# Performance work log

Hardware: AMD Instinct MI355X
Metric: run time of the kernel (lower is better)

The kernel has to match this reference:

```python
import jax, jax.numpy as jnp
import numpy as np
from jax import lax

N, OC, IC, K = 32, 256, 256, 3
H = W = 56
STRIDE = 1
PADDING = 1
SPARSITY = 0.9  # fraction of zero weights


def setup_inputs() -> dict:
    key = jax.random.key(0)
    k_in, k_w, k_b, k_m = jax.random.split(key, 4)
    input = jax.random.normal(k_in, (N, IC, H, W), dtype=jnp.float32)
    weight = jax.random.normal(k_w, (OC, IC, K, K), dtype=jnp.float32) * 0.05
    bias = jax.random.normal(k_b, (OC,), dtype=jnp.float32) * 0.05
    mask = jax.random.bernoulli(k_m, p=1.0 - SPARSITY, shape=(OC, IC, K, K))
    return {"input": input, "weight": weight, "bias": bias, "mask": mask}


def reference(input, weight, bias, mask):
    # SparseConv2d stores only nonzero weights (W_val at W_idx); mathematically this
    # is a dense conv2d with the masked weight tensor.
    w = jnp.where(mask, weight, jnp.zeros((), dtype=weight.dtype))
    out = lax.conv_general_dilated(
        input, w,
        window_strides=(STRIDE, STRIDE),
        padding=[(PADDING, PADDING), (PADDING, PADDING)],
        dimension_numbers=("NCHW", "OIHW", "NCHW"),
    )
    return out + bias[None, :, None, None]
```

## Files before the change

kernel.cpp:

```cpp
#include <hip/hip_runtime.h>

constexpr int NB=32, ICC=256, OCC=256, HH=56, WW=56;
constexpr int HW=HH*WW, CHW=ICC*HW;
constexpr int YT=14;
constexpr int BUFB = 6*58*64;
constexpr int ROWB = 58*64;
constexpr int LROW=58;
constexpr int PAD=36;
constexpr int LDS_ELEMS=6*LROW*PAD;

using short8  = __attribute__((ext_vector_type(8))) short;
using short4v = __attribute__((ext_vector_type(4))) short;
using f32x4   = __attribute__((ext_vector_type(4))) float;

__device__ inline unsigned bf16rne(float x){
  unsigned u = __float_as_uint(x);
  return (u + 0x7fffu + ((u>>16)&1u)) >> 16;
}

__global__ __launch_bounds__(256) void pack_weights(
    const float* __restrict__ w, const int* __restrict__ mask,
    unsigned short* __restrict__ wb){
  const int oc = blockIdx.x, ic = threadIdx.x;
  const int base = (oc*ICC + ic)*9;
  #pragma unroll
  for (int j=0;j<9;++j){
    float v = (mask[base+j] != 0) ? w[base+j] : 0.f;
    wb[(j*OCC + oc)*ICC + ic] = (unsigned short)bf16rne(v);
  }
}

__global__ __launch_bounds__(256) void pack_input(
    const float* __restrict__ in, unsigned short* __restrict__ inb){
  __shared__ unsigned short t[56*258];
  const int bid = blockIdx.x;
  const int n = bid/56, y = bid - n*56;
  const float* src = in + (size_t)n*CHW + y*WW;
  const int tid = threadIdx.x;
  #pragma unroll
  for (int i=0;i<14;++i){
    int idx = tid + i*256;
    int ic = idx / 14, xg = idx - ic*14;
    float4 v = *(const float4*)(src + ic*HW + xg*4);
    int xb = xg*4;
    t[(xb+0)*258 + ic] = (unsigned short)bf16rne(v.x);
    t[(xb+1)*258 + ic] = (unsigned short)bf16rne(v.y);
    t[(xb+2)*258 + ic] = (unsigned short)bf16rne(v.z);
    t[(xb+3)*258 + ic] = (unsigned short)bf16rne(v.w);
  }
  __syncthreads();
  unsigned* dst = (unsigned*)(inb + (size_t)(n*56+y)*56*256);
  #pragma unroll
  for (int i=0;i<28;++i){
    int idx = tid + i*256;
    int x = idx >> 7, icp = idx & 127;
    dst[idx] = *(const unsigned*)&t[x*258 + icp*2];
  }
}

__global__ __launch_bounds__(256,2) void conv_mfma(
    const unsigned short* __restrict__ inb, const unsigned short* __restrict__ wb,
    const float* __restrict__ bias, float* __restrict__ out){
  __shared__ unsigned short xt[2*6*58*32];

  const int lid  = blockIdx.x;
  const int xcd  = lid & 7, slot = lid >> 3;
  const int ngrp = slot / 28, rem = slot - ngrp*28;
  const int mt   = rem / 14,  yt  = rem - mt*14;
  const int n    = xcd + 8*ngrp;
  const int y0   = yt*4, ocb = mt*128;

  const int tid  = threadIdx.x;
  const int lane = tid & 63, wv = tid >> 6;
  const int q    = lane >> 4, l16 = lane & 15;

  const int ocw = ocb + (wv & 1)*64;
  const int pxw = (wv >> 1)*112;

  int base2[7][3];
  #pragma unroll
  for (int p=0;p<7;++p){
    int px = pxw + p*16 + l16;
    int yl = px / 56, x = px - yl*56;
    #pragma unroll
    for (int kw=0;kw<3;++kw){
      int c = x + kw;
      base2[p][kw] = yl*ROWB + c*64 + ((q ^ ((c>>1)&3))<<4);
    }
  }

  f32x4 acc[4][7];
  #pragma unroll
  for (int s=0;s<4;++s)
    #pragma unroll
    for (int p=0;p<7;++p) acc[s][p] = (f32x4){0.f,0.f,0.f,0.f};

  const int rskipA = (yt==0)      ? 0 : -1;
  const int rskipB = (yt==YT-1)   ? 5 : -1;

  const unsigned short* nb = inb + (size_t)n*(56*56*256);

  auto stage = [&](int buf, int ch){
    const int ic0 = ch*32;
    #pragma unroll
    for (int i=0;i<6;++i){
      int t   = wv*6 + i;
      int row = t >> 2, k = t & 3;
      if (row != rskipA && row != rskipB){
        int ir = k*64 + lane;
        int cc = ir >> 2, sub = ir & 3;
        int icg = sub ^ (((cc+1)>>1)&3);
        int y  = y0 - 1 + row;
        const unsigned short* gp = nb + (y*56 + cc)*256 + ic0 + icg*8;
        char* lp = (char*)xt + buf*BUFB + (row*58 + 1)*64 + k*1024 + lane*16;
        if (ir < 224)
          __builtin_amdgcn_global_load_lds(
              (const __attribute__((address_space(1))) void*)gp,
              (__attribute__((address_space(3))) void*)lp, 16, 0, 0);
      }
    }
  };

  auto compute = [&](int buf, int ch){
    const int ic0 = ch*32;
    const char* xb = (const char*)xt + buf*BUFB;
    const unsigned short* wpb = wb + (ocw + l16)*ICC + ic0 + q*8;
    short8 a0 = *(const short8*)(wpb          );
    short8 a1 = *(const short8*)(wpb + 16*ICC );
    short8 a2 = *(const short8*)(wpb + 32*ICC );
    short8 a3 = *(const short8*)(wpb + 48*ICC );
    __builtin_amdgcn_s_setprio(1);
    #pragma unroll
    for (int j=0;j<9;++j){
      short8 n0, n1, n2, n3;
      if (j < 8){
        const unsigned short* wn = wpb + (j+1)*OCC*ICC;
        n0 = *(const short8*)(wn          );
        n1 = *(const short8*)(wn + 16*ICC );
        n2 = *(const short8*)(wn + 32*ICC );
        n3 = *(const short8*)(wn + 48*ICC );
      }
      const int kh = j/3, kw = j - kh*3;
      const int doff = kh*ROWB;
      #pragma unroll
      for (int p=0;p<7;++p){
        short8 b = *(const short8*)(xb + base2[p][kw] + doff);
        acc[0][p] = __builtin_amdgcn_mfma_f32_16x16x32_bf16(a0, b, acc[0][p], 0,0,0);
        acc[1][p] = __builtin_amdgcn_mfma_f32_16x16x32_bf16(a1, b, acc[1][p], 0,0,0);
        acc[2][p] = __builtin_amdgcn_mfma_f32_16x16x32_bf16(a2, b, acc[2][p], 0,0,0);
        acc[3][p] = __builtin_amdgcn_mfma_f32_16x16x32_bf16(a3, b, acc[3][p], 0,0,0);
      }
      if (j < 8){ a0=n0; a1=n1; a2=n2; a3=n3; }
    }
    __builtin_amdgcn_s_setprio(0);
  };

  for (int i = tid; i < 2*BUFB/4; i += 256) ((unsigned*)xt)[i] = 0u;
  __syncthreads();

  stage(0, 0);
  __syncthreads();

  for (int ch=0; ch<8; ++ch){
    if (ch < 7) stage((ch+1)&1, ch+1);
    compute(ch&1, ch);
    __syncthreads();
  }

  #pragma unroll
  for (int s=0;s<4;++s){
    const int oc4 = ocw + s*16 + q*4;
    float4 bv = *(const float4*)(bias + oc4);
    #pragma unroll
    for (int i=0;i<4;++i){
      const float bb = (i==0)?bv.x:(i==1)?bv.y:(i==2)?bv.z:bv.w;
      float* op = out + (n*OCC + oc4 + i)*HW + y0*WW + pxw + l16;
      #pragma unroll
      for (int p=0;p<7;++p){
        op[p*16] = acc[s][p][i] + bb;
      }
    }
  }
}

__global__ __launch_bounds__(256,2) void conv_mfma_f32(
    const float* __restrict__ in, const unsigned short* __restrict__ wb,
    const float* __restrict__ bias, float* __restrict__ out){
  __shared__ unsigned short xt[LDS_ELEMS];

  const int lid  = blockIdx.x;
  const int xcd  = lid & 7, slot = lid >> 3;
  const int ngrp = slot / 28, rem = slot - ngrp*28;
  const int mt   = rem / 14,  yt  = rem - mt*14;
  const int n    = xcd + 8*ngrp;
  const int y0   = yt*4, ocb = mt*128;

  const int tid  = threadIdx.x;
  const int lane = tid & 63, wv = tid >> 6;
  const int q    = lane >> 4, l16 = lane & 15;

  for (int i = tid; i < LDS_ELEMS/2; i += 256) ((unsigned*)xt)[i] = 0u;

  const int ocw = ocb + (wv & 1)*64;
  const int pxw = (wv >> 1)*112;

  int pbase[7];
  #pragma unroll
  for (int p=0;p<7;++p){
    int px = pxw + p*16 + l16;
    int ylv = px / 56, x = px - ylv*56;
    pbase[p] = (ylv*LROW + x)*(PAD*2) + q*16;
  }

  f32x4 acc[4][7];
  #pragma unroll
  for (int s=0;s<4;++s)
    #pragma unroll
    for (int p=0;p<7;++p) acc[s][p] = (f32x4){0.f,0.f,0.f,0.f};

  const int rskipA = (yt==0)      ? 0 : -1;
  const int rskipB = (yt==YT-1)   ? 5 : -1;

  __syncthreads();

  for (int ch=0; ch<8; ++ch){
    const int ic0 = ch*32;
    #pragma unroll
    for (int i=0;i<6;++i){
      int idx = tid + i*256;
      if (idx < 1344){
        int r  = idx / 224;
        int r2 = idx - r*224;
        int xg = r2 >> 4, icp = r2 & 15;
        if (r != rskipA && r != rskipB){
          int y = y0 - 1 + r;
          const float* gp = in + n*CHW + (ic0 + icp*2)*HW + y*WW + xg*4;
          float4 g0 = *(const float4*)gp;
          float4 g1 = *(const float4*)(gp + HW);
          unsigned w0 = bf16rne(g0.x) | (bf16rne(g1.x)<<16);
          unsigned w1 = bf16rne(g0.y) | (bf16rne(g1.y)<<16);
          unsigned w2 = bf16rne(g0.z) | (bf16rne(g1.z)<<16);
          unsigned w3 = bf16rne(g0.w) | (bf16rne(g1.w)<<16);
          unsigned* dp = (unsigned*)xt + (r*LROW + 1 + xg*4)*(PAD/2) + icp;
          dp[0]         = w0;
          dp[PAD/2]     = w1;
          dp[PAD]       = w2;
          dp[3*(PAD/2)] = w3;
        }
      }
    }
    __syncthreads();

    #pragma unroll
    for (int kh=0;kh<3;++kh){
      #pragma unroll
      for (int kw=0;kw<3;++kw){
        const int j = kh*3 + kw;
        const unsigned short* wp = wb + (j*OCC + ocw + l16)*ICC + ic0 + q*8;
        short8 a0 = *(const short8*)(wp          );
        short8 a1 = *(const short8*)(wp + 16*ICC );
        short8 a2 = *(const short8*)(wp + 32*ICC );
        short8 a3 = *(const short8*)(wp + 48*ICC );
        const int doff = (kh*LROW + kw)*(PAD*2);
        #pragma unroll
        for (int p=0;p<7;++p){
          const char* bp = (const char*)xt + pbase[p] + doff;
          short4v blo = *(const short4v*)(bp    );
          short4v bhi = *(const short4v*)(bp + 8);
          short8 b = __builtin_shufflevector(blo, bhi, 0,1,2,3,4,5,6,7);
          acc[0][p] = __builtin_amdgcn_mfma_f32_16x16x32_bf16(a0, b, acc[0][p], 0,0,0);
          acc[1][p] = __builtin_amdgcn_mfma_f32_16x16x32_bf16(a1, b, acc[1][p], 0,0,0);
          acc[2][p] = __builtin_amdgcn_mfma_f32_16x16x32_bf16(a2, b, acc[2][p], 0,0,0);
          acc[3][p] = __builtin_amdgcn_mfma_f32_16x16x32_bf16(a3, b, acc[3][p], 0,0,0);
        }
      }
    }
    __syncthreads();
  }

  #pragma unroll
  for (int s=0;s<4;++s){
    const int oc4 = ocw + s*16 + q*4;
    float4 bv = *(const float4*)(bias + oc4);
    #pragma unroll
    for (int i=0;i<4;++i){
      const float bb = (i==0)?bv.x:(i==1)?bv.y:(i==2)?bv.z:bv.w;
      float* op = out + (n*OCC + oc4 + i)*HW + y0*WW + pxw + l16;
      #pragma unroll
      for (int p=0;p<7;++p){
        op[p*16] = acc[s][p][i] + bb;
      }
    }
  }
}

extern "C" void kernel_launch(void* const* d_in, const int* in_sizes, int n_in,
                              void* d_out, int out_size, void* d_ws, size_t ws_size,
                              hipStream_t stream) {
  const float* in   = (const float*)d_in[0];
  const float* w    = (const float*)d_in[1];
  const float* bias = (const float*)d_in[2];
  const int*   mask = (const int*)d_in[3];
  float*       out  = (float*)d_out;
  unsigned short* wb = (unsigned short*)d_ws;

  const size_t WB_BYTES  = (size_t)9*OCC*ICC*2;
  const size_t INB_BYTES = (size_t)NB*HH*WW*ICC*2;

  pack_weights<<<OCC, 256, 0, stream>>>(w, mask, wb);
  if (ws_size >= WB_BYTES + INB_BYTES){
    unsigned short* inb = (unsigned short*)((char*)d_ws + WB_BYTES);
    pack_input<<<NB*HH, 256, 0, stream>>>(in, inb);
    conv_mfma<<<8*4*2*YT, 256, 0, stream>>>(inb, wb, bias, out);
  } else {
    conv_mfma_f32<<<8*4*2*YT, 256, 0, stream>>>(in, wb, bias, out);
  }
}
```

Baseline: 356.8 us.

## Retile conv block to 8 output rows by 64 channels, drop weight prefetch

Each block of the bf16 MFMA conv now covers 8 output rows by 64 output channels, where it used to cover 4 rows by 128 channels. All four waves share the same channel slice and split the pixels. This cuts the halo overhead of the staged input tile (10 rows for 8 outputs instead of 6 for 4) but reloads weights twice as often per image. The weight register prefetch across taps is removed in favour of direct loads per tap, and LDS zeroing uses 16-byte stores. LDS use grows and latency hiding on weight loads may drop.

```diff
diff --git a/kernel.cpp b/kernel.cpp
--- a/kernel.cpp
+++ b/kernel.cpp
@@ -2,9 +2,10 @@
 
 constexpr int NB=32, ICC=256, OCC=256, HH=56, WW=56;
 constexpr int HW=HH*WW, CHW=ICC*HW;
+constexpr int ROWS=10;
+constexpr int BUFB = ROWS*58*64;
+constexpr int ROWB = 58*64;
 constexpr int YT=14;
-constexpr int BUFB = 6*58*64;
-constexpr int ROWB = 58*64;
 constexpr int LROW=58;
 constexpr int PAD=36;
 constexpr int LDS_ELEMS=6*LROW*PAD;
@@ -61,21 +62,20 @@
 __global__ __launch_bounds__(256,2) void conv_mfma(
     const unsigned short* __restrict__ inb, const unsigned short* __restrict__ wb,
     const float* __restrict__ bias, float* __restrict__ out){
-  __shared__ unsigned short xt[2*6*58*32];
+  __shared__ __align__(16) unsigned short xt[2*ROWS*58*32];
 
   const int lid  = blockIdx.x;
   const int xcd  = lid & 7, slot = lid >> 3;
   const int ngrp = slot / 28, rem = slot - ngrp*28;
-  const int mt   = rem / 14,  yt  = rem - mt*14;
+  const int mt   = rem / 7,  yt  = rem - mt*7;
   const int n    = xcd + 8*ngrp;
-  const int y0   = yt*4, ocb = mt*128;
+  const int y0   = yt*8, ocb = mt*64;
 
   const int tid  = threadIdx.x;
   const int lane = tid & 63, wv = tid >> 6;
   const int q    = lane >> 4, l16 = lane & 15;
 
-  const int ocw = ocb + (wv & 1)*64;
-  const int pxw = (wv >> 1)*112;
+  const int pxw = wv*112;
 
   int base2[7][3];
   #pragma unroll
@@ -95,16 +95,16 @@
     #pragma unroll
     for (int p=0;p<7;++p) acc[s][p] = (f32x4){0.f,0.f,0.f,0.f};
 
-  const int rskipA = (yt==0)      ? 0 : -1;
-  const int rskipB = (yt==YT-1)   ? 5 : -1;
+  const int rskipA = (yt==0) ? 0 : -1;
+  const int rskipB = (yt==6) ? 9 : -1;
 
   const unsigned short* nb = inb + (size_t)n*(56*56*256);
 
   auto stage = [&](int buf, int ch){
     const int ic0 = ch*32;
     #pragma unroll
-    for (int i=0;i<6;++i){
-      int t   = wv*6 + i;
+    for (int i=0;i<10;++i){
+      int t   = wv*10 + i;
       int row = t >> 2, k = t & 3;
       if (row != rskipA && row != rskipB){
         int ir = k*64 + lane;
@@ -112,7 +112,7 @@
         int icg = sub ^ (((cc+1)>>1)&3);
         int y  = y0 - 1 + row;
         const unsigned short* gp = nb + (y*56 + cc)*256 + ic0 + icg*8;
-        char* lp = (char*)xt + buf*BUFB + (row*58 + 1)*64 + k*1024 + lane*16;
+        char* lp = (char*)xt + buf*BUFB + (row*58 + 1)*64 + ir*16;
         if (ir < 224)
           __builtin_amdgcn_global_load_lds(
               (const __attribute__((address_space(1))) void*)gp,
@@ -124,22 +124,15 @@
   auto compute = [&](int buf, int ch){
     const int ic0 = ch*32;
     const char* xb = (const char*)xt + buf*BUFB;
-    const unsigned short* wpb = wb + (ocw + l16)*ICC + ic0 + q*8;
-    short8 a0 = *(const short8*)(wpb          );
-    short8 a1 = *(const short8*)(wpb + 16*ICC );
-    short8 a2 = *(const short8*)(wpb + 32*ICC );
-    short8 a3 = *(const short8*)(wpb + 48*ICC );
+    const unsigned short* wpb = wb + (ocb + l16)*ICC + ic0 + q*8;
     __builtin_amdgcn_s_setprio(1);
     #pragma unroll
     for (int j=0;j<9;++j){
-      short8 n0, n1, n2, n3;
-      if (j < 8){
-        const unsigned short* wn = wpb + (j+1)*OCC*ICC;
-        n0 = *(const short8*)(wn          );
-        n1 = *(const short8*)(wn + 16*ICC );
-        n2 = *(const short8*)(wn + 32*ICC );
-        n3 = *(const short8*)(wn + 48*ICC );
-      }
+      const unsigned short* wj = wpb + j*OCC*ICC;
+      short8 a0 = *(const short8*)(wj          );
+      short8 a1 = *(const short8*)(wj + 16*ICC );
+      short8 a2 = *(const short8*)(wj + 32*ICC );
+      short8 a3 = *(const short8*)(wj + 48*ICC );
       const int kh = j/3, kw = j - kh*3;
       const int doff = kh*ROWB;
       #pragma unroll
@@ -150,12 +143,12 @@
         acc[2][p] = __builtin_amdgcn_mfma_f32_16x16x32_bf16(a2, b, acc[2][p], 0,0,0);
         acc[3][p] = __builtin_amdgcn_mfma_f32_16x16x32_bf16(a3, b, acc[3][p], 0,0,0);
       }
-      if (j < 8){ a0=n0; a1=n1; a2=n2; a3=n3; }
     }
     __builtin_amdgcn_s_setprio(0);
   };
 
-  for (int i = tid; i < 2*BUFB/4; i += 256) ((unsigned*)xt)[i] = 0u;
+  #pragma unroll 4
+  for (int i = tid; i < 2*BUFB/16; i += 256) ((f32x4*)xt)[i] = (f32x4){0.f,0.f,0.f,0.f};
   __syncthreads();
 
   stage(0, 0);
@@ -169,7 +162,7 @@
 
   #pragma unroll
   for (int s=0;s<4;++s){
-    const int oc4 = ocw + s*16 + q*4;
+    const int oc4 = ocb + s*16 + q*4;
     float4 bv = *(const float4*)(bias + oc4);
     #pragma unroll
     for (int i=0;i<4;++i){
@@ -311,7 +304,7 @@
   if (ws_size >= WB_BYTES + INB_BYTES){
     unsigned short* inb = (unsigned short*)((char*)d_ws + WB_BYTES);
     pack_input<<<NB*HH, 256, 0, stream>>>(in, inb);
-    conv_mfma<<<8*4*2*YT, 256, 0, stream>>>(inb, wb, bias, out);
+    conv_mfma<<<8*112, 256, 0, stream>>>(inb, wb, bias, out);
   } else {
     conv_mfma_f32<<<8*4*2*YT, 256, 0, stream>>>(in, wb, bias, out);
   }
```

After: 358.1 us. Within noise of the previous version (+0.4%).

## Compute all 256 output channels per block and pack input channel pairs

Applied to the files above, without the earlier changes.

The conv kernel now computes all 256 output channels per block instead of 128, doubling per-wave accumulators to 8x7 tiles. Each staged input tile is therefore reused across twice as many MFMAs, and the number of blocks halves. The grid drops to 448 blocks at one block per CU, so fewer waves are resident and register pressure rises sharply with 224 accumulator floats per lane. The input pack kernel also packs two channels into one 32-bit LDS word to halve LDS stores, and the LDS zeroing now uses 16-byte stores.

```diff
diff --git a/kernel.cpp b/kernel.cpp
--- a/kernel.cpp
+++ b/kernel.cpp
@@ -32,21 +32,23 @@
 
 __global__ __launch_bounds__(256) void pack_input(
     const float* __restrict__ in, unsigned short* __restrict__ inb){
-  __shared__ unsigned short t[56*258];
+  __shared__ unsigned t2[56*130];
   const int bid = blockIdx.x;
   const int n = bid/56, y = bid - n*56;
   const float* src = in + (size_t)n*CHW + y*WW;
   const int tid = threadIdx.x;
   #pragma unroll
-  for (int i=0;i<14;++i){
+  for (int i=0;i<7;++i){
     int idx = tid + i*256;
-    int ic = idx / 14, xg = idx - ic*14;
-    float4 v = *(const float4*)(src + ic*HW + xg*4);
+    int icp = idx / 14, xg = idx - icp*14;
+    const float* gp = src + (2*icp)*HW + xg*4;
+    float4 g0 = *(const float4*)gp;
+    float4 g1 = *(const float4*)(gp + HW);
     int xb = xg*4;
-    t[(xb+0)*258 + ic] = (unsigned short)bf16rne(v.x);
-    t[(xb+1)*258 + ic] = (unsigned short)bf16rne(v.y);
-    t[(xb+2)*258 + ic] = (unsigned short)bf16rne(v.z);
-    t[(xb+3)*258 + ic] = (unsigned short)bf16rne(v.w);
+    t2[(xb+0)*130 + icp] = bf16rne(g0.x) | (bf16rne(g1.x)<<16);
+    t2[(xb+1)*130 + icp] = bf16rne(g0.y) | (bf16rne(g1.y)<<16);
+    t2[(xb+2)*130 + icp] = bf16rne(g0.z) | (bf16rne(g1.z)<<16);
+    t2[(xb+3)*130 + icp] = bf16rne(g0.w) | (bf16rne(g1.w)<<16);
   }
   __syncthreads();
   unsigned* dst = (unsigned*)(inb + (size_t)(n*56+y)*56*256);
@@ -54,27 +56,26 @@
   for (int i=0;i<28;++i){
     int idx = tid + i*256;
     int x = idx >> 7, icp = idx & 127;
-    dst[idx] = *(const unsigned*)&t[x*258 + icp*2];
-  }
-}
-
-__global__ __launch_bounds__(256,2) void conv_mfma(
+    dst[idx] = t2[x*130 + icp];
+  }
+}
+
+__global__ __launch_bounds__(256,1) void conv_mfma(
     const unsigned short* __restrict__ inb, const unsigned short* __restrict__ wb,
     const float* __restrict__ bias, float* __restrict__ out){
-  __shared__ unsigned short xt[2*6*58*32];
+  __shared__ __align__(16) unsigned short xt[2*6*58*32];
 
   const int lid  = blockIdx.x;
   const int xcd  = lid & 7, slot = lid >> 3;
-  const int ngrp = slot / 28, rem = slot - ngrp*28;
-  const int mt   = rem / 14,  yt  = rem - mt*14;
+  const int ngrp = slot / 14, yt = slot - ngrp*14;
   const int n    = xcd + 8*ngrp;
-  const int y0   = yt*4, ocb = mt*128;
+  const int y0   = yt*4;
 
   const int tid  = threadIdx.x;
   const int lane = tid & 63, wv = tid >> 6;
   const int q    = lane >> 4, l16 = lane & 15;
 
-  const int ocw = ocb + (wv & 1)*64;
+  const int ocw = (wv & 1)*128;
   const int pxw = (wv >> 1)*112;
 
   int base2[7][3];
@@ -89,9 +90,9 @@
     }
   }
 
-  f32x4 acc[4][7];
-  #pragma unroll
-  for (int s=0;s<4;++s)
+  f32x4 acc[8][7];
+  #pragma unroll
+  for (int s=0;s<8;++s)
     #pragma unroll
     for (int p=0;p<7;++p) acc[s][p] = (f32x4){0.f,0.f,0.f,0.f};
 
@@ -112,7 +113,7 @@
         int icg = sub ^ (((cc+1)>>1)&3);
         int y  = y0 - 1 + row;
         const unsigned short* gp = nb + (y*56 + cc)*256 + ic0 + icg*8;
-        char* lp = (char*)xt + buf*BUFB + (row*58 + 1)*64 + k*1024 + lane*16;
+        char* lp = (char*)xt + buf*BUFB + (row*58 + 1)*64 + ir*16;
         if (ir < 224)
           __builtin_amdgcn_global_load_lds(
               (const __attribute__((address_space(1))) void*)gp,
@@ -125,20 +126,27 @@
     const int ic0 = ch*32;
     const char* xb = (const char*)xt + buf*BUFB;
     const unsigned short* wpb = wb + (ocw + l16)*ICC + ic0 + q*8;
-    short8 a0 = *(const short8*)(wpb          );
-    short8 a1 = *(const short8*)(wpb + 16*ICC );
-    short8 a2 = *(const short8*)(wpb + 32*ICC );
-    short8 a3 = *(const short8*)(wpb + 48*ICC );
-    __builtin_amdgcn_s_setprio(1);
+    short8 a0 = *(const short8*)(wpb           );
+    short8 a1 = *(const short8*)(wpb +  16*ICC );
+    short8 a2 = *(const short8*)(wpb +  32*ICC );
+    short8 a3 = *(const short8*)(wpb +  48*ICC );
+    short8 a4 = *(const short8*)(wpb +  64*ICC );
+    short8 a5 = *(const short8*)(wpb +  80*ICC );
+    short8 a6 = *(const short8*)(wpb +  96*ICC );
+    short8 a7 = *(const short8*)(wpb + 112*ICC );
     #pragma unroll
     for (int j=0;j<9;++j){
-      short8 n0, n1, n2, n3;
+      short8 n0,n1,n2,n3,n4,n5,n6,n7;
       if (j < 8){
         const unsigned short* wn = wpb + (j+1)*OCC*ICC;
-        n0 = *(const short8*)(wn          );
-        n1 = *(const short8*)(wn + 16*ICC );
-        n2 = *(const short8*)(wn + 32*ICC );
-        n3 = *(const short8*)(wn + 48*ICC );
+        n0 = *(const short8*)(wn           );
+        n1 = *(const short8*)(wn +  16*ICC );
+        n2 = *(const short8*)(wn +  32*ICC );
+        n3 = *(const short8*)(wn +  48*ICC );
+        n4 = *(const short8*)(wn +  64*ICC );
+        n5 = *(const short8*)(wn +  80*ICC );
+        n6 = *(const short8*)(wn +  96*ICC );
+        n7 = *(const short8*)(wn + 112*ICC );
       }
       const int kh = j/3, kw = j - kh*3;
       const int doff = kh*ROWB;
@@ -149,13 +157,17 @@
         acc[1][p] = __builtin_amdgcn_mfma_f32_16x16x32_bf16(a1, b, acc[1][p], 0,0,0);
         acc[2][p] = __builtin_amdgcn_mfma_f32_16x16x32_bf16(a2, b, acc[2][p], 0,0,0);
         acc[3][p] = __builtin_amdgcn_mfma_f32_16x16x32_bf16(a3, b, acc[3][p], 0,0,0);
-      }
-      if (j < 8){ a0=n0; a1=n1; a2=n2; a3=n3; }
-    }
-    __builtin_amdgcn_s_setprio(0);
+        acc[4][p] = __builtin_amdgcn_mfma_f32_16x16x32_bf16(a4, b, acc[4][p], 0,0,0);
+        acc[5][p] = __builtin_amdgcn_mfma_f32_16x16x32_bf16(a5, b, acc[5][p], 0,0,0);
+        acc[6][p] = __builtin_amdgcn_mfma_f32_16x16x32_bf16(a6, b, acc[6][p], 0,0,0);
+        acc[7][p] = __builtin_amdgcn_mfma_f32_16x16x32_bf16(a7, b, acc[7][p], 0,0,0);
+      }
+      if (j < 8){ a0=n0;a1=n1;a2=n2;a3=n3;a4=n4;a5=n5;a6=n6;a7=n7; }
+    }
   };
 
-  for (int i = tid; i < 2*BUFB/4; i += 256) ((unsigned*)xt)[i] = 0u;
+  #pragma unroll 4
+  for (int i = tid; i < 2*BUFB/16; i += 256) ((f32x4*)xt)[i] = (f32x4){0.f,0.f,0.f,0.f};
   __syncthreads();
 
   stage(0, 0);
@@ -168,7 +180,7 @@
   }
 
   #pragma unroll
-  for (int s=0;s<4;++s){
+  for (int s=0;s<8;++s){
     const int oc4 = ocw + s*16 + q*4;
     float4 bv = *(const float4*)(bias + oc4);
     #pragma unroll
@@ -311,7 +323,7 @@
   if (ws_size >= WB_BYTES + INB_BYTES){
     unsigned short* inb = (unsigned short*)((char*)d_ws + WB_BYTES);
     pack_input<<<NB*HH, 256, 0, stream>>>(in, inb);
-    conv_mfma<<<8*4*2*YT, 256, 0, stream>>>(inb, wb, bias, out);
+    conv_mfma<<<8*56, 256, 0, stream>>>(inb, wb, bias, out);
   } else {
     conv_mfma_f32<<<8*4*2*YT, 256, 0, stream>>>(in, wb, bias, out);
   }
```

New measurement: 385.9 us. +8.2%, slower.
